# Kernel tuning notes

Measured on AMD Instinct MI355X. Metric: run time of the kernel, lower is better.

## Reference

```python
import jax, jax.numpy as jnp
import numpy as np

N_NODES = 100000


def _degree_norms(src, dst, n):
    ones = jnp.ones(src.shape[0], dtype=jnp.float32)
    deg_out = jax.ops.segment_sum(ones, src, num_segments=n)
    deg_in = jax.ops.segment_sum(ones, dst, num_segments=n)
    norm_src = jnp.where(deg_out > 0, jax.lax.rsqrt(jnp.maximum(deg_out, 1.0)), 0.0)
    norm_dst = jnp.where(deg_in > 0, jax.lax.rsqrt(jnp.maximum(deg_in, 1.0)), 0.0)
    return norm_src, norm_dst


def _gcn_layer(x, W, b, src, dst, norm_src, norm_dst, n):
    # DGL GraphConv norm='both': D_dst^{-1/2} A D_src^{-1/2} X W + b
    h = (x * norm_src[:, None]) @ W          # [N, d_out]
    agg = jax.ops.segment_sum(h[src], dst, num_segments=n)  # SpMM gather/scatter
    return agg * norm_dst[:, None] + b


def setup_inputs() -> dict:
    key = jax.random.key(0)
    ks = jax.random.split(key, 8)
    E = 1600000
    x = jax.random.normal(ks[0], (N_NODES, 128), dtype=jnp.float32)
    edge_index = jax.random.randint(ks[1], (2, E), 0, N_NODES, dtype=jnp.int64)
    s = 1.0 / np.sqrt(128.0)
    W1 = jax.random.uniform(ks[2], (128, 128), jnp.float32, -s, s)
    b1 = jnp.zeros((128,), jnp.float32)
    W2 = jax.random.uniform(ks[3], (128, 128), jnp.float32, -s, s)
    b2 = jnp.zeros((128,), jnp.float32)
    W3 = jax.random.uniform(ks[4], (128, 256), jnp.float32, -s, s)
    b3 = jnp.zeros((256,), jnp.float32)
    return {"x": x, "edge_index": edge_index, "W1": W1, "b1": b1,
            "W2": W2, "b2": b2, "W3": W3, "b3": b3}


def reference(x, edge_index, W1, b1, W2, b2, W3, b3):
    src, dst = edge_index[0], edge_index[1]
    norm_src, norm_dst = _degree_norms(src, dst, N_NODES)
    h = jax.nn.relu(_gcn_layer(x, W1, b1, src, dst, norm_src, norm_dst, N_NODES))
    h = jax.nn.relu(_gcn_layer(h, W2, b2, src, dst, norm_src, norm_dst, N_NODES))
    h = _gcn_layer(h, W3, b3, src, dst, norm_src, norm_dst, N_NODES)
    return (h, edge_index)
```

## Files before the change

kernel.cpp:

```cpp
#include <hip/hip_runtime.h>

typedef _Float16 f16;
typedef _Float16 f16x8 __attribute__((ext_vector_type(8)));
typedef float f32x2 __attribute__((ext_vector_type(2)));
typedef float f32x4 __attribute__((ext_vector_type(4)));
typedef int i32x4 __attribute__((ext_vector_type(4)));

#define ROWB 1024
#define OFF_AGG 0
#define OFF_SA 256
#define OFF_SB 384
#define OFF_K 512
#define OFF_ADJ 768

__device__ __forceinline__ float bf2f(unsigned short h) {
  return __uint_as_float(((unsigned)h) << 16);
}
__device__ __forceinline__ unsigned short f2bf(float f) {
  unsigned u = __float_as_uint(f);
  u += 0x7fffu + ((u >> 16) & 1u);
  return (unsigned short)(u >> 16);
}
__device__ __forceinline__ float scrub(float v) {
  if (!(v == v)) return 0.f;
  return fminf(fmaxf(v, -65504.f), 65504.f);
}
__device__ __forceinline__ float scrub8(float v) {
  if (!(v == v)) return 0.f;
  return fminf(fmaxf(v, -240.f), 240.f);
}
__device__ __forceinline__ int iclamp(int v, int lo, int hi) {
  return v < lo ? lo : (v > hi ? hi : v);
}
__device__ __forceinline__ int adj_read(const char* H, int i) {
  return *(const int*)(H + ((size_t)(i >> 6)) * ROWB + OFF_ADJ + (i & 63) * 4);
}
__device__ __forceinline__ void adj_write(char* H, int i, int v) {
  *(int*)(H + ((size_t)(i >> 6)) * ROWB + OFF_ADJ + (i & 63) * 4) = v;
}
__device__ __forceinline__ int enc4(float a, float b, float c, float d) {
  int w = __builtin_amdgcn_cvt_pk_fp8_f32(a, b, 0, false);
  w = __builtin_amdgcn_cvt_pk_fp8_f32(c, d, w, true);
  return w;
}
__device__ __forceinline__ void dec_acc(i32x4 w, float* acc, float sc) {
#pragma unroll
  for (int d = 0; d < 4; ++d) {
    f32x2 lo = __builtin_amdgcn_cvt_pk_f32_fp8(w[d], false);
    f32x2 hi = __builtin_amdgcn_cvt_pk_f32_fp8(w[d], true);
    acc[d * 4 + 0] += sc * lo[0];
    acc[d * 4 + 1] += sc * lo[1];
    acc[d * 4 + 2] += sc * hi[0];
    acc[d * 4 + 3] += sc * hi[1];
  }
}

__global__ __launch_bounds__(64) void k_detect(const int* __restrict__ ei,
                                               int* __restrict__ flag) {
  int lane = threadIdx.x;
  int v = ei[2 * lane + 1];
  unsigned long long m = __ballot(v == 0);
  if (lane == 0) *flag = (m == 0xFFFFFFFFFFFFFFFFull) ? 1 : 0;
}

__global__ __launch_bounds__(256) void k_degree_edges(const int* __restrict__ ei, int E,
                                                      int n, const int* __restrict__ flag,
                                                      unsigned* __restrict__ dego,
                                                      unsigned* __restrict__ degi,
                                                      float* __restrict__ eout,
                                                      char* __restrict__ H, int gd) {
  const int sh = *flag;
  const int tid = threadIdx.x;
  if ((int)blockIdx.x < gd) {
    const int base = blockIdx.x * 1536 + tid;
#pragma unroll
    for (int k = 0; k < 6; ++k) {
      int e = base + k * 256;
      if (e < E) {
        int s = iclamp(ei[(size_t)e << sh], 0, n - 1);
        int d = iclamp(ei[((size_t)E << sh) + ((size_t)e << sh)], 0, n - 1);
        atomicAdd(&dego[s], 1u);
        int rk = (int)atomicAdd(&degi[d], 1u);
        *(int*)(H + ((size_t)(e >> 6)) * ROWB + OFF_K + (e & 63) * 4) = rk;
      }
    }
  } else {
    const int m = 2 * E;
    const int base = (blockIdx.x - gd) * 1024 + tid;
#pragma unroll
    for (int k = 0; k < 4; ++k) {
      int i = base + k * 256;
      if (i < m) {
        int v = ei[(size_t)i << sh];
        eout[i] = bf2f(f2bf((float)v));
      }
    }
  }
}

__global__ __launch_bounds__(256) void k_scan1(const int* __restrict__ deg, int n,
                                               int* __restrict__ bsum) {
  __shared__ int sh[256];
  int tid = threadIdx.x;
  int i = blockIdx.x * 256 + tid;
  sh[tid] = (i < n) ? deg[i] : 0;
  __syncthreads();
  for (int s = 128; s > 0; s >>= 1) {
    if (tid < s) sh[tid] += sh[tid + s];
    __syncthreads();
  }
  if (tid == 0) bsum[blockIdx.x] = sh[0];
}

__global__ __launch_bounds__(512) void k_scan2(int* __restrict__ bsum, int nb,
                                               int* __restrict__ total_out) {
  __shared__ int sh[512];
  int tid = threadIdx.x;
  int v = (tid < nb) ? bsum[tid] : 0;
  sh[tid] = v;
  __syncthreads();
  for (int off = 1; off < 512; off <<= 1) {
    int t = (tid >= off) ? sh[tid - off] : 0;
    __syncthreads();
    sh[tid] += t;
    __syncthreads();
  }
  if (tid < nb) bsum[tid] = sh[tid] - v;
  if (tid == 0) *total_out = sh[511];
}

__global__ __launch_bounds__(256) void k_scan3(const int* __restrict__ deg,
                                               const int* __restrict__ bsum,
                                               int* __restrict__ rowptr, int n) {
  __shared__ int sh[256];
  int tid = threadIdx.x;
  int i = blockIdx.x * 256 + tid;
  int v = (i < n) ? deg[i] : 0;
  sh[tid] = v;
  __syncthreads();
  for (int off = 1; off < 256; off <<= 1) {
    int t = (tid >= off) ? sh[tid - off] : 0;
    __syncthreads();
    sh[tid] += t;
    __syncthreads();
  }
  if (i < n) rowptr[i] = bsum[blockIdx.x] + sh[tid] - v;
}

__global__ __launch_bounds__(256) void k_fill_normscale(const int* __restrict__ ei, int E,
                                                        int n, const int* __restrict__ flag,
                                                        const int* __restrict__ rowptr,
                                                        unsigned* __restrict__ dego,
                                                        unsigned* __restrict__ degi,
                                                        const float* __restrict__ X,
                                                        char* __restrict__ H, int gf) {
  __shared__ float ns[256];
  const int tid = threadIdx.x;
  if ((int)blockIdx.x < gf) {
    const int sh = *flag;
    const int base = blockIdx.x * 1024 + tid;
#pragma unroll
    for (int k = 0; k < 4; ++k) {
      int e = base + k * 256;
      if (e < E) {
        int s = iclamp(ei[(size_t)e << sh], 0, n - 1);
        int d = iclamp(ei[((size_t)E << sh) + ((size_t)e << sh)], 0, n - 1);
        int rk = *(const int*)(H + ((size_t)(e >> 6)) * ROWB + OFF_K + (e & 63) * 4);
        int idx = iclamp(rowptr[d] + rk, 0, E - 1);
        adj_write(H, idx, s);
      }
    }
  } else {
    const int rb = (blockIdx.x - gf) * 256;
    int r = rb + tid;
    float f = 0.f;
    if (r < n) {
      unsigned a = dego[r];
      f = a ? rsqrtf((float)a) : 0.f;
      dego[r] = __float_as_uint(f);
      unsigned b = degi[r];
      degi[r] = __float_as_uint(b ? rsqrtf((float)b) : 0.f);
    }
    ns[tid] = f;
    __syncthreads();
    const int nrow = (n - rb < 256) ? (n - rb) : 256;
    for (int q = tid; q < nrow * 32; q += 256) {
      int lr = q >> 5, c = q & 31;
      int row = rb + lr;
      float4 v = ((const float4*)X)[(size_t)row * 32 + c];
      float s = ns[lr];
      int w = enc4(scrub8(v.x * s), scrub8(v.y * s), scrub8(v.z * s), scrub8(v.w * s));
      *(int*)(H + (size_t)row * ROWB + OFF_SB + c * 4) = w;
    }
  }
}

__global__ __launch_bounds__(256) void k_aggregate(const char* __restrict__ H,
                                                   int sinOff,
                                                   const int* __restrict__ rowptr,
                                                   const unsigned* __restrict__ ndst,
                                                   int n, int E) {
  const int wv = blockIdx.x * 4 + (threadIdx.x >> 6);
  const int lane = threadIdx.x & 63;
  const int gw0 = wv * 2, gw1 = gw0 + 1;
  if (gw0 >= n) return;
  int s0 = iclamp(rowptr[gw0], 0, E);
  int e0 = iclamp(rowptr[gw0 + 1], s0, E);
  const bool has1 = (gw1 < n);
  int s1 = has1 ? iclamp(rowptr[gw1], 0, E) : 0;
  int e1 = has1 ? iclamp(rowptr[gw1 + 1], s1, E) : 0;
  const char* Sin = H + sinOff;
  const int grp = lane >> 3;
  const int sub = lane & 7;
  float a0[16] = {}, a1[16] = {};
  int i0 = s0, i1 = s1;
  while (i0 + 8 <= e0 && i1 + 8 <= e1) {
    int nA = iclamp(adj_read(H, i0 + grp), 0, n - 1);
    int nB = iclamp(adj_read(H, i1 + grp), 0, n - 1);
    i32x4 wA = *(const i32x4*)(Sin + (size_t)nA * ROWB + sub * 16);
    i32x4 wB = *(const i32x4*)(Sin + (size_t)nB * ROWB + sub * 16);
    dec_acc(wA, a0, 1.f);
    dec_acc(wB, a1, 1.f);
    i0 += 8;
    i1 += 8;
  }
  for (; i0 + 8 <= e0; i0 += 8) {
    int nA = iclamp(adj_read(H, i0 + grp), 0, n - 1);
    i32x4 wA = *(const i32x4*)(Sin + (size_t)nA * ROWB + sub * 16);
    dec_acc(wA, a0, 1.f);
  }
  for (; i1 + 8 <= e1; i1 += 8) {
    int nB = iclamp(adj_read(H, i1 + grp), 0, n - 1);
    i32x4 wB = *(const i32x4*)(Sin + (size_t)nB * ROWB + sub * 16);
    dec_acc(wB, a1, 1.f);
  }
  for (; i0 < e0; i0 += 8) {
    int idx = i0 + grp;
    float sc = (idx < e0) ? 1.f : 0.f;
    int nb = iclamp(adj_read(H, idx < e0 ? idx : i0), 0, n - 1);
    i32x4 w = *(const i32x4*)(Sin + (size_t)nb * ROWB + sub * 16);
    dec_acc(w, a0, sc);
  }
  for (; i1 < e1; i1 += 8) {
    int idx = i1 + grp;
    float sc = (idx < e1) ? 1.f : 0.f;
    int nb = iclamp(adj_read(H, idx < e1 ? idx : i1), 0, n - 1);
    i32x4 w = *(const i32x4*)(Sin + (size_t)nb * ROWB + sub * 16);
    dec_acc(w, a1, sc);
  }
#pragma unroll
  for (int j = 0; j < 16; ++j) {
    a0[j] += __shfl_xor(a0[j], 8, 64);
    a0[j] += __shfl_xor(a0[j], 16, 64);
    a0[j] += __shfl_xor(a0[j], 32, 64);
    a1[j] += __shfl_xor(a1[j], 8, 64);
    a1[j] += __shfl_xor(a1[j], 16, 64);
    a1[j] += __shfl_xor(a1[j], 32, 64);
  }
  if (lane < 8) {
    float nd = __uint_as_float(ndst[gw0]);
    f16x8 o0, o1;
#pragma unroll
    for (int j = 0; j < 8; ++j) {
      o0[j] = (f16)scrub(a0[j] * nd);
      o1[j] = (f16)scrub(a0[8 + j] * nd);
    }
    char* dst = ((char*)H) + OFF_AGG + (size_t)gw0 * ROWB + lane * 32;
    *(f16x8*)dst = o0;
    *(f16x8*)(dst + 16) = o1;
  } else if (lane < 16 && has1) {
    int l = lane & 7;
    float nd = __uint_as_float(ndst[gw1]);
    f16x8 o0, o1;
#pragma unroll
    for (int j = 0; j < 8; ++j) {
      o0[j] = (f16)scrub(a1[j] * nd);
      o1[j] = (f16)scrub(a1[8 + j] * nd);
    }
    char* dst = ((char*)H) + OFF_AGG + (size_t)gw1 * ROWB + l * 32;
    *(f16x8*)dst = o0;
    *(f16x8*)(dst + 16) = o1;
  }
}

template <int DOUT, bool MID>
__global__ __launch_bounds__(256) void k_gemm(const char* __restrict__ A,
                                              const float* __restrict__ W,
                                              const float* __restrict__ bias,
                                              const unsigned* __restrict__ nsrc,
                                              char* __restrict__ OUT, int n) {
  extern __shared__ char smem_raw[];
  f16* sB = (f16*)smem_raw;
  const int tid = threadIdx.x;
  for (int idx = tid; idx < 128 * DOUT; idx += 256) {
    int k = idx / DOUT;
    int nn = idx % DOUT;
    int g = (k >> 3) ^ (nn & 15);
    sB[nn * 128 + (g << 3) + (k & 7)] = (f16)scrub(W[idx]);
  }
  __syncthreads();
  const int wave = tid >> 6, lane = tid & 63;
  const int quad = lane >> 4, l16 = lane & 15;
  const int rowbase = blockIdx.x * 128 + wave * 32;
  constexpr int NT = DOUT / 16;
  f32x4 acc[2][NT] = {};
  int r0 = rowbase + l16;      if (r0 > n - 1) r0 = n - 1;
  int r1 = rowbase + 16 + l16; if (r1 > n - 1) r1 = n - 1;
#pragma unroll
  for (int ks = 0; ks < 4; ++ks) {
    const int k0 = ks * 32 + quad * 8;
    const int kg = ks * 4 + quad;
    f16x8 a0 = *(const f16x8*)(A + (size_t)r0 * ROWB + k0 * 2);
    f16x8 a1 = *(const f16x8*)(A + (size_t)r1 * ROWB + k0 * 2);
#pragma unroll
    for (int nt = 0; nt < NT; ++nt) {
      int nn = nt * 16 + l16;
      f16x8 b = *(const f16x8*)(sB + nn * 128 + ((kg ^ l16) << 3));
      acc[0][nt] = __builtin_amdgcn_mfma_f32_16x16x32_f16(a0, b, acc[0][nt], 0, 0, 0);
      acc[1][nt] = __builtin_amdgcn_mfma_f32_16x16x32_f16(a1, b, acc[1][nt], 0, 0, 0);
    }
  }
#pragma unroll
  for (int mt = 0; mt < 2; ++mt) {
#pragma unroll
    for (int r = 0; r < 4; ++r) {
      int row = rowbase + mt * 16 + quad * 4 + r;
      if (row >= n) continue;
      float ns = MID ? __uint_as_float(nsrc[row]) : 1.f;
#pragma unroll
      for (int nt = 0; nt < NT; ++nt) {
        int col = nt * 16 + l16;
        float v = acc[mt][nt][r] + bias[col];
        if (MID) {
          v = fminf(fmaxf(v, 0.f) * ns, 240.f);
          if (!(v == v)) v = 0.f;
          int w8 = __builtin_amdgcn_cvt_pk_fp8_f32(v, v, 0, false);
          *(unsigned char*)(OUT + (size_t)row * ROWB + col) = (unsigned char)(w8 & 0xff);
        } else {
          *(float*)(OUT + (size_t)row * ROWB + col * 4) = scrub(v);
        }
      }
    }
  }
}

extern "C" void kernel_launch(void* const* d_in, const int* in_sizes, int n_in,
                              void* d_out, int out_size, void* d_ws, size_t ws_size,
                              hipStream_t stream) {
  const float* X = (const float*)d_in[0];
  const int* EI = (const int*)d_in[1];
  const float* W1 = (const float*)d_in[2];
  const float* B1 = (const float*)d_in[3];
  const float* W2 = (const float*)d_in[4];
  const float* B2 = (const float*)d_in[5];
  const float* W3 = (const float*)d_in[6];
  const float* B3 = (const float*)d_in[7];

  const int n = in_sizes[0] / 128;
  const int E = in_sizes[1] / 2;

  char* w = (char*)d_ws;
  const size_t nb = ((size_t)n * 4 + 1023) & ~(size_t)1023;
  int* flag        = (int*)(w);
  unsigned* dego   = (unsigned*)(w + 1024);
  unsigned* degi   = (unsigned*)(w + 1024 + nb);
  int* rowptr      = (int*)(w + 1024 + 2 * nb);
  int* bsum        = (int*)(w + 1024 + 3 * nb);

  char* H = (char*)d_out;

  const int gd = (E + 1535) / 1536;
  const int ge = (2 * E + 1023) / 1024;
  const int gf = (E + 1023) / 1024;
  const int gN = (n + 255) / 256;
  const int g2 = (n + 7) / 8;
  const int gG = (n + 127) / 128;

  hipMemsetAsync(dego, 0, (size_t)n * 4, stream);
  hipMemsetAsync(degi, 0, (size_t)n * 4, stream);

  k_detect<<<1, 64, 0, stream>>>(EI, flag);
  k_degree_edges<<<gd + ge, 256, 0, stream>>>(EI, E, n, flag, dego, degi,
                                              (float*)d_out + (size_t)n * 256, H, gd);
  k_scan1<<<gN, 256, 0, stream>>>((const int*)degi, n, bsum);
  k_scan2<<<1, 512, 0, stream>>>(bsum, gN, rowptr + n);
  k_scan3<<<gN, 256, 0, stream>>>((const int*)degi, bsum, rowptr, n);
  k_fill_normscale<<<gf + gN, 256, 0, stream>>>(EI, E, n, flag, rowptr, dego, degi,
                                                X, H, gf);

  k_aggregate<<<g2, 256, 0, stream>>>(H, OFF_SB, rowptr, degi, n, E);
  k_gemm<128, true><<<gG, 256, 128 * 128 * 2, stream>>>(H + OFF_AGG, W1, B1, dego,
                                                        H + OFF_SA, n);
  k_aggregate<<<g2, 256, 0, stream>>>(H, OFF_SA, rowptr, degi, n, E);
  k_gemm<128, true><<<gG, 256, 128 * 128 * 2, stream>>>(H + OFF_AGG, W2, B2, dego,
                                                        H + OFF_SB, n);
  k_aggregate<<<g2, 256, 0, stream>>>(H, OFF_SB, rowptr, degi, n, E);
  k_gemm<256, false><<<gG, 256, 256 * 128 * 2, stream>>>(H + OFF_AGG, W3, B3, dego,
                                                         H, n);
}
```

Measured before the change: 679.3 us.

## Build CSR via two-level bucket sort with shared-memory histograms instead of global atomics

New measurement: 642.1 us. 5.5% less time.

```diff
diff --git a/kernel.cpp b/kernel.cpp
--- a/kernel.cpp
+++ b/kernel.cpp
@@ -10,7 +10,6 @@
 #define OFF_AGG 0
 #define OFF_SA 256
 #define OFF_SB 384
-#define OFF_K 512
 #define OFF_ADJ 768
 
 __device__ __forceinline__ float bf2f(unsigned short h) {
@@ -37,6 +36,21 @@
 }
 __device__ __forceinline__ void adj_write(char* H, int i, int v) {
   *(int*)(H + ((size_t)(i >> 6)) * ROWB + OFF_ADJ + (i & 63) * 4) = v;
+}
+__device__ __forceinline__ int cread(const char* H, size_t base, int i) {
+  return *(const int*)(H + base + ((size_t)(i >> 7)) * ROWB + (i & 127) * 4);
+}
+__device__ __forceinline__ i32x4 cread4(const char* H, size_t base, int i) {
+  return *(const i32x4*)(H + base + ((size_t)(i >> 7)) * ROWB + (i & 127) * 4);
+}
+__device__ __forceinline__ void cwrite(char* H, size_t base, int i, int v) {
+  *(int*)(H + base + ((size_t)(i >> 7)) * ROWB + (i & 127) * 4) = v;
+}
+__device__ __forceinline__ int2 pread(const char* H, size_t base, int i) {
+  return *(const int2*)(H + base + ((size_t)(i >> 6)) * ROWB + (i & 63) * 8);
+}
+__device__ __forceinline__ void pwrite(char* H, size_t base, int i, int2 v) {
+  *(int2*)(H + base + ((size_t)(i >> 6)) * ROWB + (i & 63) * 8) = v;
 }
 __device__ __forceinline__ int enc4(float a, float b, float c, float d) {
   int w = __builtin_amdgcn_cvt_pk_fp8_f32(a, b, 0, false);
@@ -63,39 +77,137 @@
   if (lane == 0) *flag = (m == 0xFFFFFFFFFFFFFFFFull) ? 1 : 0;
 }
 
-__global__ __launch_bounds__(256) void k_degree_edges(const int* __restrict__ ei, int E,
-                                                      int n, const int* __restrict__ flag,
-                                                      unsigned* __restrict__ dego,
-                                                      unsigned* __restrict__ degi,
-                                                      float* __restrict__ eout,
-                                                      char* __restrict__ H, int gd) {
+__global__ __launch_bounds__(256) void k_compact(const int* __restrict__ ei, int E,
+                                                 int n, const int* __restrict__ flag,
+                                                 char* __restrict__ H, size_t srcB,
+                                                 size_t dstB, float* __restrict__ eout) {
   const int sh = *flag;
   const int tid = threadIdx.x;
-  if ((int)blockIdx.x < gd) {
-    const int base = blockIdx.x * 1536 + tid;
-#pragma unroll
-    for (int k = 0; k < 6; ++k) {
-      int e = base + k * 256;
-      if (e < E) {
-        int s = iclamp(ei[(size_t)e << sh], 0, n - 1);
-        int d = iclamp(ei[((size_t)E << sh) + ((size_t)e << sh)], 0, n - 1);
-        atomicAdd(&dego[s], 1u);
-        int rk = (int)atomicAdd(&degi[d], 1u);
-        *(int*)(H + ((size_t)(e >> 6)) * ROWB + OFF_K + (e & 63) * 4) = rk;
-      }
-    }
-  } else {
-    const int m = 2 * E;
-    const int base = (blockIdx.x - gd) * 1024 + tid;
+  const int base = blockIdx.x * 1024 + tid;
+  const int m = 2 * E;
+#pragma unroll
+  for (int k = 0; k < 4; ++k) {
+    int i = base + k * 256;
+    if (i < m) {
+      int v = ei[(size_t)i << sh];
+      eout[i] = bf2f(f2bf((float)v));
+      int c = iclamp(v, 0, n - 1);
+      if (i < E) cwrite(H, srcB, i, c);
+      else cwrite(H, dstB, i - E, c);
+    }
+  }
+}
+
+__global__ __launch_bounds__(256) void k_coarse(char* __restrict__ H, size_t dstB,
+                                                size_t cB, int E, int R, int CE) {
+  __shared__ unsigned c[64];
+  const int tid = threadIdx.x;
+  if (tid < 64) c[tid] = 0;
+  __syncthreads();
+  const int lo = blockIdx.x * CE, hi = min(lo + CE, E);
+  for (int i = lo + tid; i < hi; i += 256) {
+    unsigned d = (unsigned)cread(H, dstB, i);
+    atomicAdd(&c[d / (unsigned)R], 1u);
+  }
+  __syncthreads();
+  if (tid < 64) cwrite(H, cB, tid * 256 + (int)blockIdx.x, (int)c[tid]);
+}
+
+__global__ __launch_bounds__(1024) void k_cscan(char* __restrict__ H, size_t cB) {
+  __shared__ int bs[1024];
+  const int tid = threadIdx.x;
+  const int per = 16;
+  const int base = tid * per;
+  int vals[16];
+  int sum = 0;
+#pragma unroll
+  for (int j = 0; j < per; ++j) {
+    vals[j] = cread(H, cB, base + j);
+    sum += vals[j];
+  }
+  bs[tid] = sum;
+  __syncthreads();
+  for (int off = 1; off < 1024; off <<= 1) {
+    int t = (tid >= off) ? bs[tid - off] : 0;
+    __syncthreads();
+    bs[tid] += t;
+    __syncthreads();
+  }
+  int ex = bs[tid] - sum;
+#pragma unroll
+  for (int j = 0; j < per; ++j) {
+    int v = vals[j];
+    cwrite(H, cB, base + j, ex);
+    ex += v;
+  }
+}
+
+__global__ __launch_bounds__(256) void k_bucket(char* __restrict__ H, size_t srcB,
+                                                size_t dstB, size_t cB, size_t pB,
+                                                int E, int R, int CE) {
+  __shared__ int cu[64];
+  const int tid = threadIdx.x;
+  if (tid < 64) cu[tid] = cread(H, cB, tid * 256 + (int)blockIdx.x);
+  __syncthreads();
+  const int lo = blockIdx.x * CE, hi = min(lo + CE, E);
+  for (int i = lo + tid; i < hi; i += 256) {
+    int s = cread(H, srcB, i);
+    int d = cread(H, dstB, i);
+    int pos = atomicAdd(&cu[(unsigned)d / (unsigned)R], 1);
+    pwrite(H, pB, pos, make_int2(s, d));
+  }
+}
+
+__global__ __launch_bounds__(512) void k_hsrc(char* __restrict__ H, size_t srcB,
+                                              size_t poB, int NPAD, int n, int E, int R) {
+  extern __shared__ unsigned hh[];
+  const int r = blockIdx.x >> 2, sl = blockIdx.x & 3;
+  const int lo = r * R;
+  if (lo >= n) return;
+  const int hi = min(lo + R, n);
+  const int tid = threadIdx.x;
+  for (int j = tid; j < R; j += 512) hh[j] = 0;
+  __syncthreads();
+  int ES = (((E + 3) / 4) + 3) & ~3;
+  const int s0 = sl * ES, s1 = min(s0 + ES, E);
+  const int span = (unsigned)(hi - lo);
+  const int m4 = s0 + ((s1 - s0) & ~3);
+  for (int i = s0 + tid * 4; i < m4; i += 2048) {
+    i32x4 v = cread4(H, srcB, i);
 #pragma unroll
     for (int k = 0; k < 4; ++k) {
-      int i = base + k * 256;
-      if (i < m) {
-        int v = ei[(size_t)i << sh];
-        eout[i] = bf2f(f2bf((float)v));
-      }
-    }
-  }
+      unsigned u = (unsigned)(v[k] - lo);
+      if (u < (unsigned)span) atomicAdd(&hh[u], 1u);
+    }
+  }
+  for (int i = m4 + tid; i < s1; i += 512) {
+    unsigned u = (unsigned)(cread(H, srcB, i) - lo);
+    if (u < (unsigned)span) atomicAdd(&hh[u], 1u);
+  }
+  __syncthreads();
+  for (int j = tid; j < hi - lo; j += 512) cwrite(H, poB, sl * NPAD + lo + j, (int)hh[j]);
+}
+
+__global__ __launch_bounds__(1024) void k_hdst(char* __restrict__ H, size_t pB,
+                                               size_t cB, unsigned* __restrict__ degi,
+                                               int n, int E, int R) {
+  extern __shared__ unsigned hh2[];
+  const int r = blockIdx.x;
+  const int lo = r * R;
+  if (lo >= n) return;
+  const int hi = min(lo + R, n);
+  const int tid = threadIdx.x;
+  for (int j = tid; j < R; j += 1024) hh2[j] = 0;
+  __syncthreads();
+  const int b0 = cread(H, cB, r * 256);
+  const int b1 = (r == (int)gridDim.x - 1) ? E : cread(H, cB, (r + 1) * 256);
+  for (int i = b0 + tid; i < b1; i += 1024) {
+    int2 p = pread(H, pB, i);
+    unsigned u = (unsigned)(p.y - lo);
+    if (u < (unsigned)(hi - lo)) atomicAdd(&hh2[u], 1u);
+  }
+  __syncthreads();
+  for (int j = tid; j < hi - lo; j += 1024) degi[lo + j] = hh2[j];
 }
 
 __global__ __launch_bounds__(256) void k_scan1(const int* __restrict__ deg, int n,
@@ -147,51 +259,66 @@
   if (i < n) rowptr[i] = bsum[blockIdx.x] + sh[tid] - v;
 }
 
-__global__ __launch_bounds__(256) void k_fill_normscale(const int* __restrict__ ei, int E,
-                                                        int n, const int* __restrict__ flag,
-                                                        const int* __restrict__ rowptr,
-                                                        unsigned* __restrict__ dego,
-                                                        unsigned* __restrict__ degi,
-                                                        const float* __restrict__ X,
-                                                        char* __restrict__ H, int gf) {
+__global__ __launch_bounds__(1024) void k_fillp(char* __restrict__ H, size_t pB,
+                                                size_t cB, const int* __restrict__ rowptr,
+                                                int n, int E, int R, int CAP) {
+  extern __shared__ int sm[];
+  int* cur = sm;
+  int* stg = sm + R;
+  const int r = blockIdx.x;
+  const int lo = r * R;
+  if (lo >= n) return;
+  const int hi = min(lo + R, n);
+  const int tid = threadIdx.x;
+  const int segBase = rowptr[lo];
+  const int segEnd = rowptr[hi];
+  for (int j = tid; j < hi - lo; j += 1024) cur[j] = rowptr[lo + j] - segBase;
+  __syncthreads();
+  const int b0 = cread(H, cB, r * 256);
+  const int b1 = (r == (int)gridDim.x - 1) ? E : cread(H, cB, (r + 1) * 256);
+  for (int i = b0 + tid; i < b1; i += 1024) {
+    int2 p = pread(H, pB, i);
+    unsigned u = (unsigned)(p.y - lo);
+    if (u < (unsigned)(hi - lo)) {
+      int slot = atomicAdd(&cur[u], 1);
+      if (slot < CAP) stg[slot] = p.x;
+      else adj_write(H, iclamp(segBase + slot, 0, E - 1), p.x);
+    }
+  }
+  __syncthreads();
+  int m = segEnd - segBase;
+  if (m > CAP) m = CAP;
+  for (int j = tid; j < m; j += 1024) adj_write(H, segBase + j, stg[j]);
+}
+
+__global__ __launch_bounds__(256) void k_normscale(char* __restrict__ H, size_t poB,
+                                                   int NPAD, unsigned* __restrict__ dego,
+                                                   unsigned* __restrict__ degi,
+                                                   const float* __restrict__ X, int n) {
   __shared__ float ns[256];
   const int tid = threadIdx.x;
-  if ((int)blockIdx.x < gf) {
-    const int sh = *flag;
-    const int base = blockIdx.x * 1024 + tid;
-#pragma unroll
-    for (int k = 0; k < 4; ++k) {
-      int e = base + k * 256;
-      if (e < E) {
-        int s = iclamp(ei[(size_t)e << sh], 0, n - 1);
-        int d = iclamp(ei[((size_t)E << sh) + ((size_t)e << sh)], 0, n - 1);
-        int rk = *(const int*)(H + ((size_t)(e >> 6)) * ROWB + OFF_K + (e & 63) * 4);
-        int idx = iclamp(rowptr[d] + rk, 0, E - 1);
-        adj_write(H, idx, s);
-      }
-    }
-  } else {
-    const int rb = (blockIdx.x - gf) * 256;
-    int r = rb + tid;
-    float f = 0.f;
-    if (r < n) {
-      unsigned a = dego[r];
-      f = a ? rsqrtf((float)a) : 0.f;
-      dego[r] = __float_as_uint(f);
-      unsigned b = degi[r];
-      degi[r] = __float_as_uint(b ? rsqrtf((float)b) : 0.f);
-    }
-    ns[tid] = f;
-    __syncthreads();
-    const int nrow = (n - rb < 256) ? (n - rb) : 256;
-    for (int q = tid; q < nrow * 32; q += 256) {
-      int lr = q >> 5, c = q & 31;
-      int row = rb + lr;
-      float4 v = ((const float4*)X)[(size_t)row * 32 + c];
-      float s = ns[lr];
-      int w = enc4(scrub8(v.x * s), scrub8(v.y * s), scrub8(v.z * s), scrub8(v.w * s));
-      *(int*)(H + (size_t)row * ROWB + OFF_SB + c * 4) = w;
-    }
+  const int rb = blockIdx.x * 256;
+  int r = rb + tid;
+  float f = 0.f;
+  if (r < n) {
+    unsigned a = 0;
+#pragma unroll
+    for (int s = 0; s < 4; ++s) a += (unsigned)cread(H, poB, s * NPAD + r);
+    f = a ? rsqrtf((float)a) : 0.f;
+    dego[r] = __float_as_uint(f);
+    unsigned b = degi[r];
+    degi[r] = __float_as_uint(b ? rsqrtf((float)b) : 0.f);
+  }
+  ns[tid] = f;
+  __syncthreads();
+  const int nrow = (n - rb < 256) ? (n - rb) : 256;
+  for (int q = tid; q < nrow * 32; q += 256) {
+    int lr = q >> 5, c = q & 31;
+    int row = rb + lr;
+    float4 v = ((const float4*)X)[(size_t)row * 32 + c];
+    float s = ns[lr];
+    int w = enc4(scrub8(v.x * s), scrub8(v.y * s), scrub8(v.z * s), scrub8(v.w * s));
+    *(int*)(H + (size_t)row * ROWB + OFF_SB + c * 4) = w;
   }
 }
 
@@ -369,24 +496,41 @@
 
   char* H = (char*)d_out;
 
-  const int gd = (E + 1535) / 1536;
-  const int ge = (2 * E + 1023) / 1024;
-  const int gf = (E + 1023) / 1024;
+  const int kRows  = (E + 63) / 64;
+  const int cR32   = (E + 127) / 128;
+  const int pRows  = (E + 63) / 64;
+  const int poRows = (n + 127) / 128;
+  const int NPAD   = poRows * 128;
+  const size_t srcB = (size_t)kRows * ROWB + 512;
+  const size_t dstB = srcB + (size_t)cR32 * ROWB;
+  const size_t pB   = dstB + (size_t)cR32 * ROWB;
+  const size_t poB  = pB + (size_t)pRows * ROWB;
+  const size_t cB   = poB + (size_t)4 * poRows * ROWB;
+
+  const int R  = (n + 63) / 64;
+  const int NR = 64;
+  const int NB = 256;
+  const int CE = (E + NB - 1) / NB;
+  const int CAP = 28672;
+
+  const int gc = (2 * E + 1023) / 1024;
   const int gN = (n + 255) / 256;
   const int g2 = (n + 7) / 8;
   const int gG = (n + 127) / 128;
 
-  hipMemsetAsync(dego, 0, (size_t)n * 4, stream);
-  hipMemsetAsync(degi, 0, (size_t)n * 4, stream);
-
   k_detect<<<1, 64, 0, stream>>>(EI, flag);
-  k_degree_edges<<<gd + ge, 256, 0, stream>>>(EI, E, n, flag, dego, degi,
-                                              (float*)d_out + (size_t)n * 256, H, gd);
+  k_compact<<<gc, 256, 0, stream>>>(EI, E, n, flag, H, srcB, dstB,
+                                    (float*)d_out + (size_t)n * 256);
+  k_coarse<<<NB, 256, 0, stream>>>(H, dstB, cB, E, R, CE);
+  k_cscan<<<1, 1024, 0, stream>>>(H, cB);
+  k_bucket<<<NB, 256, 0, stream>>>(H, srcB, dstB, cB, pB, E, R, CE);
+  k_hsrc<<<NR * 4, 512, (size_t)R * 4, stream>>>(H, srcB, poB, NPAD, n, E, R);
+  k_hdst<<<NR, 1024, (size_t)R * 4, stream>>>(H, pB, cB, degi, n, E, R);
   k_scan1<<<gN, 256, 0, stream>>>((const int*)degi, n, bsum);
   k_scan2<<<1, 512, 0, stream>>>(bsum, gN, rowptr + n);
   k_scan3<<<gN, 256, 0, stream>>>((const int*)degi, bsum, rowptr, n);
-  k_fill_normscale<<<gf + gN, 256, 0, stream>>>(EI, E, n, flag, rowptr, dego, degi,
-                                                X, H, gf);
+  k_fillp<<<NR, 1024, (size_t)(R + CAP) * 4, stream>>>(H, pB, cB, rowptr, n, E, R, CAP);
+  k_normscale<<<gN, 256, 0, stream>>>(H, poB, NPAD, dego, degi, X, n);
 
   k_aggregate<<<g2, 256, 0, stream>>>(H, OFF_SB, rowptr, degi, n, E);
   k_gemm<128, true><<<gG, 256, 128 * 128 * 2, stream>>>(H + OFF_AGG, W1, B1, dego,
```
